# Performance work log

Hardware: AMD Instinct MI355X
Metric: run time of the kernel (lower is better)

The kernel has to match this reference:

```python
import jax, jax.numpy as jnp
import numpy as np

N_NODES = 100000
N_EDGES = 1600000
D_IN, D_HID, D_OUT = 128, 128, 64


def spmm(row, col, val, h, n):
    # y[i] = sum_{e: row[e]==i} val[e] * h[col[e]]  (A_hat @ h with A in COO form)
    return jax.ops.segment_sum(val[:, None] * h[col], row, num_segments=n)


def setup_inputs() -> dict:
    key = jax.random.key(0)
    ks = jax.random.split(key, 7)
    x = jax.random.normal(ks[0], (1, N_NODES, D_IN), dtype=jnp.float32)
    edge_row = jax.random.randint(ks[1], (N_EDGES,), 0, N_NODES, dtype=jnp.int32)
    edge_col = jax.random.randint(ks[2], (N_EDGES,), 0, N_NODES, dtype=jnp.int32)
    edge_val = jax.random.uniform(ks[3], (N_EDGES,), dtype=jnp.float32)
    W0 = jax.random.normal(ks[4], (D_HID, D_IN), dtype=jnp.float32) * 0.05
    W1 = jax.random.normal(ks[5], (D_HID, D_HID), dtype=jnp.float32) * 0.05
    W2 = jax.random.normal(ks[6], (D_OUT, D_HID), dtype=jnp.float32) * 0.05
    return {"x": x, "edge_row": edge_row, "edge_col": edge_col,
            "edge_val": edge_val, "W0": W0, "W1": W1, "W2": W2}


def reference(x, edge_row, edge_col, edge_val, W0, W1, W2):
    B, N, D = x.shape
    n = B * N
    h = x.reshape(n, D)
    # input conv: Linear (no bias) -> SpMM -> ReLU
    h = jax.nn.relu(spmm(edge_row, edge_col, edge_val, h @ W0.T, n))
    # hidden conv with residual: ReLU(A (h W1^T)) + h
    h = jax.nn.relu(spmm(edge_row, edge_col, edge_val, h @ W1.T, n)) + h
    # dropout is identity in eval mode
    out = spmm(edge_row, edge_col, edge_val, h @ W2.T, n)
    return out
```

## Files before the change

### kernel.cpp

```cpp
#include <hip/hip_runtime.h>


typedef unsigned int u32;
typedef unsigned short u16;
typedef __attribute__((ext_vector_type(8))) short bf16x8;
typedef __attribute__((ext_vector_type(4))) float f32x4;

constexpr int NN = 100000;
constexpr int NE = 1600000;
constexpr int PAD = 100352;
constexpr int NBUCK = 392;
constexpr int BCAP = 4608;
constexpr int EPB = 4096;
constexpr int P1B = (NE + EPB - 1) / EPB;
constexpr int G0B = (NN + 63) / 64;
constexpr int EPT = BCAP / 256;
constexpr int NPASS = 13;

__device__ __forceinline__ u16 f2bf(float f) {
    u32 x = __float_as_uint(f);
    x += 0x7fffu + ((x >> 16) & 1u);
    return (u16)(x >> 16);
}

__device__ __forceinline__ void wfrag_one(const float* __restrict__ W,
                                          u16* __restrict__ Wf, int total, int i)
{
    if (i < total) {
        const int j    = i & 7;
        const int lane = (i >> 3) & 63;
        const int kc   = (i >> 9) & 3;
        const int ct   = i >> 11;
        const int src  = (ct * 16 + (lane & 15)) * 128 + kc * 32 + (lane >> 4) * 8 + j;
        Wf[i] = f2bf(W[src]);
    }
}

__global__ __launch_bounds__(256)
void wcvt_kernel(const float* __restrict__ W0, const float* __restrict__ W1,
                 const float* __restrict__ W2, u16* __restrict__ wf0,
                 u16* __restrict__ wf1, u16* __restrict__ wf2,
                 int* __restrict__ bcur)
{
    const int i = blockIdx.x * 256 + threadIdx.x;
    if (i < 512) bcur[i] = 0;
    wfrag_one(W0, wf0, 128 * 128, i);
    wfrag_one(W1, wf1, 128 * 128, i);
    wfrag_one(W2, wf2, 64 * 128, i);
}

__global__ __launch_bounds__(256)
void k1_kernel(const float* __restrict__ x, const u16* __restrict__ Wf,
               u16* __restrict__ Cb,
               const int* __restrict__ erow, const int* __restrict__ ecol,
               const float* __restrict__ eval, int* __restrict__ bcur,
               int2* __restrict__ part)
{
    __shared__ u16 smem[64 * 136];
    const int tid = threadIdx.x;

    if ((int)blockIdx.x < P1B) {
        int* shist = (int*)smem;
        int* sbase = shist + NBUCK;
        for (int i = tid; i < NBUCK; i += 256) shist[i] = 0;
        __syncthreads();

        const int base = blockIdx.x * EPB;
        #pragma unroll
        for (int j = 0; j < EPB / 256; ++j) {
            const int e = base + j * 256 + tid;
            if (e < NE) atomicAdd(&shist[erow[e] >> 8], 1);
        }
        __syncthreads();
        for (int i = tid; i < NBUCK; i += 256) {
            const int c = shist[i];
            sbase[i] = c ? atomicAdd(&bcur[i], c) : 0;
            shist[i] = 0;
        }
        __syncthreads();
        #pragma unroll
        for (int j = 0; j < EPB / 256; ++j) {
            const int e = base + j * 256 + tid;
            if (e < NE) {
                const int r = erow[e];
                const int b = r >> 8;
                const int rk = atomicAdd(&shist[b], 1);
                part[(size_t)b * BCAP + sbase[b] + rk] =
                    make_int2(((r & 255) << 17) | ecol[e], __float_as_int(eval[e]));
            }
        }
        return;
    }

    constexpr int RS   = 136;
    constexpr int PADW = 136;
    u16* sA = smem;
    u16* sC = smem;
    const int w    = tid >> 6;
    const int lane = tid & 63;
    const int m    = lane & 15;
    const int q    = lane >> 4;
    const int rowBase = ((int)blockIdx.x - P1B) * 64;

    #pragma unroll
    for (int i = 0; i < 8; ++i) {
        const int g = (i * 256 + tid) * 4;
        const int r = g >> 7, c = g & 127;
        float4 v = make_float4(0.f, 0.f, 0.f, 0.f);
        if (rowBase + r < NN) v = *(const float4*)(x + (size_t)(rowBase + r) * 128 + c);
        u16* d = &sA[r * RS + c];
        d[0] = f2bf(v.x); d[1] = f2bf(v.y); d[2] = f2bf(v.z); d[3] = f2bf(v.w);
    }
    __syncthreads();

    bf16x8 afrag[4];
    #pragma unroll
    for (int kc = 0; kc < 4; ++kc)
        afrag[kc] = *(const bf16x8*)&sA[(w * 16 + m) * RS + kc * 32 + q * 8];
    __syncthreads();

    #pragma unroll
    for (int ct = 0; ct < 8; ++ct) {
        f32x4 acc = {0.f, 0.f, 0.f, 0.f};
        #pragma unroll
        for (int kc = 0; kc < 4; ++kc) {
            const bf16x8 b = *(const bf16x8*)(Wf + (((ct * 4 + kc) * 64) + lane) * 8);
            acc = __builtin_amdgcn_mfma_f32_16x16x32_bf16(afrag[kc], b, acc, 0, 0, 0);
        }
        #pragma unroll
        for (int r = 0; r < 4; ++r)
            sC[(w * 16 + q * 4 + r) * PADW + ct * 16 + m] = f2bf(acc[r]);
    }
    __syncthreads();

    const int g    = lane >> 2;
    const int cb   = (lane & 3) * 32;
    const int grow = rowBase + w * 16 + g;
    if (grow < NN) {
        #pragma unroll
        for (int i = 0; i < 4; ++i) {
            const int4 v = *(const int4*)&sC[(w * 16 + g) * PADW + cb + i * 8];
            *(int4*)(Cb + (size_t)grow * 128 + cb + i * 8) = v;
        }
    }
}

__global__ __launch_bounds__(256)
void part2_kernel(const int* __restrict__ bcur, const int2* __restrict__ part,
                  int* __restrict__ offs, int2* __restrict__ pce)
{
    __shared__ int scnt[256];
    __shared__ int rowoff[256];
    __shared__ int sdata[256];
    __shared__ int2 sout[BCAP];
    const int b = blockIdx.x;
    const int tid = threadIdx.x;

    const int cnt = bcur[b];
    const int2* src = part + (size_t)b * BCAP;

    int2 ed[EPT];
    #pragma unroll
    for (int j = 0; j < EPT; ++j) {
        const int idx = j * 256 + tid;
        ed[j] = (idx < cnt) ? src[idx] : make_int2(-1, 0);
    }

    int partial = 0;
    for (int i = tid; i < b; i += 256) partial += bcur[i];
    sdata[tid] = partial;
    __syncthreads();
    #pragma unroll
    for (int off = 128; off > 0; off >>= 1) {
        if (tid < off) sdata[tid] += sdata[tid + off];
        __syncthreads();
    }
    const int gb = sdata[0];
    __syncthreads();

    scnt[tid] = 0;
    __syncthreads();
    #pragma unroll
    for (int j = 0; j < EPT; ++j)
        if (ed[j].x >= 0) atomicAdd(&scnt[((u32)ed[j].x) >> 17], 1);
    __syncthreads();

    const int c = scnt[tid];
    sdata[tid] = c;
    __syncthreads();
    #pragma unroll
    for (int off = 1; off < 256; off <<= 1) {
        const int val = (tid >= off) ? sdata[tid - off] : 0;
        __syncthreads();
        sdata[tid] += val;
        __syncthreads();
    }
    const int excl = sdata[tid] - c;
    rowoff[tid] = excl;
    offs[b * 256 + tid] = gb + excl;
    __syncthreads();

    for (int p = 0; p < NPASS; ++p) {
        #pragma unroll
        for (int j = 0; j < EPT; ++j) {
            const int key = ed[j].x & 0x1FFFF;
            if ((key >> 13) == p) {
                const int rl  = ((u32)ed[j].x) >> 17;
                const int pos = atomicAdd(&rowoff[rl], 1);
                sout[pos] = make_int2(key, ed[j].y);
            }
        }
        __syncthreads();
    }

    #pragma unroll
    for (int j = 0; j < EPT; ++j) {
        const int idx = j * 256 + tid;
        if (idx < cnt) pce[(size_t)gb + idx] = sout[idx];
    }
}

template<int LPC>
__device__ __forceinline__ void load_row(const u16* p, u32* u) {
    if constexpr (LPC == 8) {
        const uint4 t = *(const uint4*)p;
        u[0] = t.x; u[1] = t.y; u[2] = t.z; u[3] = t.w;
    } else {
        const uint2 t = *(const uint2*)p;
        u[0] = t.x; u[1] = t.y;
    }
}

template<int LPC>
__device__ __forceinline__ void fma_row(float v, const u32* u, float* a) {
    #pragma unroll
    for (int j = 0; j < LPC / 2; ++j) {
        a[2*j]   = fmaf(v, __uint_as_float(u[j] << 16),         a[2*j]);
        a[2*j+1] = fmaf(v, __uint_as_float(u[j] & 0xffff0000u), a[2*j+1]);
    }
}

template<int DO, int MODE>
__global__ __launch_bounds__(256)
void spmm_gemm(const int* __restrict__ offs, const int2* __restrict__ pce,
               const u16* __restrict__ Hb, const u16* __restrict__ Wf,
               const u16* __restrict__ Res, u16* __restrict__ Cb,
               u16* __restrict__ Hout)
{
    constexpr int RS   = 136;
    constexpr int PADW = DO + 8;
    __shared__ u16 smem[16 * 136];
    const int tid = threadIdx.x;
    const int ln  = tid & 15;
    const int rl  = tid >> 4;
    const int row = blockIdx.x * 16 + rl;

    const int s = offs[row];
    const int t = offs[row + 1];
    const u16* hbase = Hb + ln * 8;

    float a0[8], a1[8];
    #pragma unroll
    for (int j = 0; j < 8; ++j) { a0[j] = 0.f; a1[j] = 0.f; }

    int e = s;
    for (; e + 1 < t; e += 2) {
        const int2 e0 = pce[e];
        const int2 e1 = pce[e + 1];
        u32 u0[4], u1[4];
        load_row<8>(hbase + (size_t)e0.x * 128, u0);
        load_row<8>(hbase + (size_t)e1.x * 128, u1);
        fma_row<8>(__int_as_float(e0.y), u0, a0);
        fma_row<8>(__int_as_float(e1.y), u1, a1);
    }
    if (e < t) {
        const int2 e0 = pce[e];
        u32 u0[4];
        load_row<8>(hbase + (size_t)e0.x * 128, u0);
        fma_row<8>(__int_as_float(e0.y), u0, a0);
    }
    #pragma unroll
    for (int j = 0; j < 8; ++j) a0[j] = fmaxf(a0[j] + a1[j], 0.f);

    if constexpr (MODE == 2) {
        u32 r[4];
        load_row<8>(Res + (size_t)row * 128 + ln * 8, r);
        #pragma unroll
        for (int j = 0; j < 4; ++j) {
            a0[2*j]   += __uint_as_float(r[j] << 16);
            a0[2*j+1] += __uint_as_float(r[j] & 0xffff0000u);
        }
    }
    u32 o[4];
    #pragma unroll
    for (int j = 0; j < 4; ++j)
        o[j] = (u32)f2bf(a0[2*j]) | ((u32)f2bf(a0[2*j+1]) << 16);
    const uint4 packed = make_uint4(o[0], o[1], o[2], o[3]);
    *(uint4*)&smem[rl * RS + ln * 8] = packed;
    if constexpr (MODE == 1)
        *(uint4*)(Hout + (size_t)row * 128 + ln * 8) = packed;
    __syncthreads();

    constexpr int TPW = DO / 64;
    const int w    = tid >> 6;
    const int lane = tid & 63;
    const int m    = lane & 15;
    const int q    = lane >> 4;

    bf16x8 afrag[4];
    #pragma unroll
    for (int kc = 0; kc < 4; ++kc)
        afrag[kc] = *(const bf16x8*)&smem[m * RS + kc * 32 + q * 8];

    f32x4 acc[TPW];
    #pragma unroll
    for (int tw = 0; tw < TPW; ++tw) {
        const int ct = w * TPW + tw;
        acc[tw] = (f32x4){0.f, 0.f, 0.f, 0.f};
        #pragma unroll
        for (int kc = 0; kc < 4; ++kc) {
            const bf16x8 b = *(const bf16x8*)(Wf + (((ct * 4 + kc) * 64) + lane) * 8);
            acc[tw] = __builtin_amdgcn_mfma_f32_16x16x32_bf16(afrag[kc], b, acc[tw], 0, 0, 0);
        }
    }
    __syncthreads();

    #pragma unroll
    for (int tw = 0; tw < TPW; ++tw) {
        const int ct = w * TPW + tw;
        #pragma unroll
        for (int r = 0; r < 4; ++r)
            smem[(q * 4 + r) * PADW + ct * 16 + m] = f2bf(acc[tw][r]);
    }
    __syncthreads();

    if (DO == 128 || tid < 128) {
        const int g = tid * 8;
        const int r = g / DO;
        const int c = g % DO;
        const int4 v = *(const int4*)&smem[r * PADW + c];
        *(int4*)(Cb + ((size_t)blockIdx.x * 16 + r) * DO + c) = v;
    }
}

__global__ __launch_bounds__(256)
void spmm_out(const int* __restrict__ offs, const int2* __restrict__ pce,
              const u16* __restrict__ Hb, float* __restrict__ Y)
{
    const int ln  = threadIdx.x & 15;
    const int row = blockIdx.x * 16 + (threadIdx.x >> 4);
    if (row >= NN) return;
    const int s = offs[row];
    const int t = offs[row + 1];
    const u16* hbase = Hb + ln * 4;

    float a0[4], a1[4];
    #pragma unroll
    for (int j = 0; j < 4; ++j) { a0[j] = 0.f; a1[j] = 0.f; }

    int e = s;
    for (; e + 1 < t; e += 2) {
        const int2 e0 = pce[e];
        const int2 e1 = pce[e + 1];
        u32 u0[2], u1[2];
        load_row<4>(hbase + (size_t)e0.x * 64, u0);
        load_row<4>(hbase + (size_t)e1.x * 64, u1);
        fma_row<4>(__int_as_float(e0.y), u0, a0);
        fma_row<4>(__int_as_float(e1.y), u1, a1);
    }
    if (e < t) {
        const int2 e0 = pce[e];
        u32 u0[2];
        load_row<4>(hbase + (size_t)e0.x * 64, u0);
        fma_row<4>(__int_as_float(e0.y), u0, a0);
    }
    #pragma unroll
    for (int j = 0; j < 4; ++j) a0[j] += a1[j];
    *(float4*)(Y + (size_t)row * 64 + ln * 4) = make_float4(a0[0], a0[1], a0[2], a0[3]);
}

extern "C" void kernel_launch(void* const* d_in, const int* in_sizes, int n_in,
                              void* d_out, int out_size, void* d_ws, size_t ws_size,
                              hipStream_t stream) {
    const float* x    = (const float*)d_in[0];
    const int*   erow = (const int*)  d_in[1];
    const int*   ecol = (const int*)  d_in[2];
    const float* eval = (const float*)d_in[3];
    const float* W0   = (const float*)d_in[4];
    const float* W1   = (const float*)d_in[5];
    const float* W2   = (const float*)d_in[6];
    float* out = (float*)d_out;

    char* p = (char*)d_ws;
    const size_t BUFB = (size_t)NN * 128 * sizeof(u16);
    u16* t0b  = (u16*)p;  p += BUFB;
    u16* t1b  = (u16*)p;  p += BUFB;
    u16* h1b  = (u16*)p;  p += BUFB;
    u16* wf0  = (u16*)p;  p += 128 * 128 * 2;
    u16* wf1  = (u16*)p;  p += 128 * 128 * 2;
    u16* wf2  = (u16*)p;  p += 64 * 128 * 2;
    int* bcur   = (int*)p; p += 512 * 4;
    int* offs   = (int*)p; p += ((size_t)PAD + 256) * 4;
    int2* part  = (int2*)p; p += (size_t)NBUCK * BCAP * 8;
    int2* pce   = (int2*)p;

    const dim3 blk(256);
    const int rowBlocks = NN / 16;

    wcvt_kernel<<<64, blk, 0, stream>>>(W0, W1, W2, wf0, wf1, wf2, bcur);
    k1_kernel  <<<P1B + G0B, blk, 0, stream>>>(x, wf0, t0b, erow, ecol, eval, bcur, part);
    part2_kernel<<<NBUCK, blk, 0, stream>>>(bcur, part, offs, pce);
    spmm_gemm<128, 1><<<rowBlocks, blk, 0, stream>>>(offs, pce, t0b, wf1, nullptr, t1b, h1b);
    spmm_gemm<64, 2><<<rowBlocks, blk, 0, stream>>>(offs, pce, t1b, wf2, h1b, t0b, nullptr);
    spmm_out<<<rowBlocks, blk, 0, stream>>>(offs, pce, t0b, out);
}
```

Baseline: 357.3 us.

## Replace multi-pass bucket scatter with per-row column-bucket counting sort; unroll SpMM gather by four

The partition kernel used to scatter edges in 13 sequential passes, each over all edges with a barrier in between, to order edges by column bucket within a row. It now counts per (row, column-bucket) pair in shared memory, builds offsets with a prefix sum, and scatters every edge in a single pass. The SpMM gather loops also process four edges per iteration, putting more independent loads in flight. This costs more shared memory (256×13 counters) and more registers in the SpMM kernels, which may lower occupancy.

```diff
diff --git a/kernel.cpp b/kernel.cpp
--- a/kernel.cpp
+++ b/kernel.cpp
@@ -15,7 +15,7 @@
 constexpr int P1B = (NE + EPB - 1) / EPB;
 constexpr int G0B = (NN + 63) / 64;
 constexpr int EPT = BCAP / 256;
-constexpr int NPASS = 13;
+constexpr int NCB = 13;
 
 __device__ __forceinline__ u16 f2bf(float f) {
     u32 x = __float_as_uint(f);
@@ -149,8 +149,7 @@
 void part2_kernel(const int* __restrict__ bcur, const int2* __restrict__ part,
                   int* __restrict__ offs, int2* __restrict__ pce)
 {
-    __shared__ int scnt[256];
-    __shared__ int rowoff[256];
+    __shared__ int scnt[256 * NCB];
     __shared__ int sdata[256];
     __shared__ int2 sout[BCAP];
     const int b = blockIdx.x;
@@ -166,6 +165,9 @@
         ed[j] = (idx < cnt) ? src[idx] : make_int2(-1, 0);
     }
 
+    #pragma unroll
+    for (int j = 0; j < NCB; ++j) scnt[j * 256 + tid] = 0;
+
     int partial = 0;
     for (int i = tid; i < b; i += 256) partial += bcur[i];
     sdata[tid] = partial;
@@ -178,15 +180,20 @@
     const int gb = sdata[0];
     __syncthreads();
 
-    scnt[tid] = 0;
-    __syncthreads();
-    #pragma unroll
-    for (int j = 0; j < EPT; ++j)
-        if (ed[j].x >= 0) atomicAdd(&scnt[((u32)ed[j].x) >> 17], 1);
-    __syncthreads();
-
-    const int c = scnt[tid];
-    sdata[tid] = c;
+    #pragma unroll
+    for (int j = 0; j < EPT; ++j) {
+        if (ed[j].x >= 0) {
+            const int rl = ((u32)ed[j].x) >> 17;
+            const int cb = (ed[j].x & 0x1FFFF) >> 13;
+            atomicAdd(&scnt[rl * NCB + cb], 1);
+        }
+    }
+    __syncthreads();
+
+    int rsum = 0;
+    #pragma unroll
+    for (int j = 0; j < NCB; ++j) rsum += scnt[tid * NCB + j];
+    sdata[tid] = rsum;
     __syncthreads();
     #pragma unroll
     for (int off = 1; off < 256; off <<= 1) {
@@ -195,23 +202,28 @@
         sdata[tid] += val;
         __syncthreads();
     }
-    const int excl = sdata[tid] - c;
-    rowoff[tid] = excl;
+    const int excl = sdata[tid] - rsum;
     offs[b * 256 + tid] = gb + excl;
-    __syncthreads();
-
-    for (int p = 0; p < NPASS; ++p) {
-        #pragma unroll
-        for (int j = 0; j < EPT; ++j) {
-            const int key = ed[j].x & 0x1FFFF;
-            if ((key >> 13) == p) {
-                const int rl  = ((u32)ed[j].x) >> 17;
-                const int pos = atomicAdd(&rowoff[rl], 1);
-                sout[pos] = make_int2(key, ed[j].y);
-            }
-        }
-        __syncthreads();
-    }
+
+    int run = excl;
+    #pragma unroll
+    for (int j = 0; j < NCB; ++j) {
+        const int c = scnt[tid * NCB + j];
+        scnt[tid * NCB + j] = run;
+        run += c;
+    }
+    __syncthreads();
+
+    #pragma unroll
+    for (int j = 0; j < EPT; ++j) {
+        if (ed[j].x >= 0) {
+            const int rl  = ((u32)ed[j].x) >> 17;
+            const int cb  = (ed[j].x & 0x1FFFF) >> 13;
+            const int pos = atomicAdd(&scnt[rl * NCB + cb], 1);
+            sout[pos] = make_int2(ed[j].x & 0x1FFFF, ed[j].y);
+        }
+    }
+    __syncthreads();
 
     #pragma unroll
     for (int j = 0; j < EPT; ++j) {
@@ -264,20 +276,35 @@
     for (int j = 0; j < 8; ++j) { a0[j] = 0.f; a1[j] = 0.f; }
 
     int e = s;
+    for (; e + 3 < t; e += 4) {
+        const int2 E0 = pce[e];
+        const int2 E1 = pce[e + 1];
+        const int2 E2 = pce[e + 2];
+        const int2 E3 = pce[e + 3];
+        u32 u0[4], u1[4], u2[4], u3[4];
+        load_row<8>(hbase + (size_t)E0.x * 128, u0);
+        load_row<8>(hbase + (size_t)E1.x * 128, u1);
+        load_row<8>(hbase + (size_t)E2.x * 128, u2);
+        load_row<8>(hbase + (size_t)E3.x * 128, u3);
+        fma_row<8>(__int_as_float(E0.y), u0, a0);
+        fma_row<8>(__int_as_float(E1.y), u1, a1);
+        fma_row<8>(__int_as_float(E2.y), u2, a0);
+        fma_row<8>(__int_as_float(E3.y), u3, a1);
+    }
     for (; e + 1 < t; e += 2) {
-        const int2 e0 = pce[e];
-        const int2 e1 = pce[e + 1];
+        const int2 E0 = pce[e];
+        const int2 E1 = pce[e + 1];
         u32 u0[4], u1[4];
-        load_row<8>(hbase + (size_t)e0.x * 128, u0);
-        load_row<8>(hbase + (size_t)e1.x * 128, u1);
-        fma_row<8>(__int_as_float(e0.y), u0, a0);
-        fma_row<8>(__int_as_float(e1.y), u1, a1);
+        load_row<8>(hbase + (size_t)E0.x * 128, u0);
+        load_row<8>(hbase + (size_t)E1.x * 128, u1);
+        fma_row<8>(__int_as_float(E0.y), u0, a0);
+        fma_row<8>(__int_as_float(E1.y), u1, a1);
     }
     if (e < t) {
-        const int2 e0 = pce[e];
+        const int2 E0 = pce[e];
         u32 u0[4];
-        load_row<8>(hbase + (size_t)e0.x * 128, u0);
-        fma_row<8>(__int_as_float(e0.y), u0, a0);
+        load_row<8>(hbase + (size_t)E0.x * 128, u0);
+        fma_row<8>(__int_as_float(E0.y), u0, a0);
     }
     #pragma unroll
     for (int j = 0; j < 8; ++j) a0[j] = fmaxf(a0[j] + a1[j], 0.f);
@@ -359,20 +386,35 @@
     for (int j = 0; j < 4; ++j) { a0[j] = 0.f; a1[j] = 0.f; }
 
     int e = s;
+    for (; e + 3 < t; e += 4) {
+        const int2 E0 = pce[e];
+        const int2 E1 = pce[e + 1];
+        const int2 E2 = pce[e + 2];
+        const int2 E3 = pce[e + 3];
+        u32 u0[2], u1[2], u2[2], u3[2];
+        load_row<4>(hbase + (size_t)E0.x * 64, u0);
+        load_row<4>(hbase + (size_t)E1.x * 64, u1);
+        load_row<4>(hbase + (size_t)E2.x * 64, u2);
+        load_row<4>(hbase + (size_t)E3.x * 64, u3);
+        fma_row<4>(__int_as_float(E0.y), u0, a0);
+        fma_row<4>(__int_as_float(E1.y), u1, a1);
+        fma_row<4>(__int_as_float(E2.y), u2, a0);
+        fma_row<4>(__int_as_float(E3.y), u3, a1);
+    }
     for (; e + 1 < t; e += 2) {
-        const int2 e0 = pce[e];
-        const int2 e1 = pce[e + 1];
+        const int2 E0 = pce[e];
+        const int2 E1 = pce[e + 1];
         u32 u0[2], u1[2];
-        load_row<4>(hbase + (size_t)e0.x * 64, u0);
-        load_row<4>(hbase + (size_t)e1.x * 64, u1);
-        fma_row<4>(__int_as_float(e0.y), u0, a0);
-        fma_row<4>(__int_as_float(e1.y), u1, a1);
+        load_row<4>(hbase + (size_t)E0.x * 64, u0);
+        load_row<4>(hbase + (size_t)E1.x * 64, u1);
+        fma_row<4>(__int_as_float(E0.y), u0, a0);
+        fma_row<4>(__int_as_float(E1.y), u1, a1);
     }
     if (e < t) {
-        const int2 e0 = pce[e];
+        const int2 E0 = pce[e];
         u32 u0[2];
-        load_row<4>(hbase + (size_t)e0.x * 64, u0);
-        fma_row<4>(__int_as_float(e0.y), u0, a0);
+        load_row<4>(hbase + (size_t)E0.x * 64, u0);
+        fma_row<4>(__int_as_float(E0.y), u0, a0);
     }
     #pragma unroll
     for (int j = 0; j < 4; ++j) a0[j] += a1[j];
```

Result: faster. 329.3 us (-7.9%).
